# Optimization experiments

Measured on AMD Instinct MI355X. Metric: run time of the kernel, lower is better.

## Reference

```python
import jax, jax.numpy as jnp
import numpy as np

CODEBOOK_SIZE = 2048
LATENT_DIM = 256
COMMITMENT_BETA = 0.25
B, C, T = 16, LATENT_DIM, 2048


def setup_inputs() -> dict:
    key = jax.random.key(0)
    k1, k2 = jax.random.split(key)
    x = jax.random.normal(k1, (B, C, T), dtype=jnp.float32)
    # matches nn.Embedding.weight.data.uniform_(-1/K, 1/K)
    codebook = jax.random.uniform(
        k2, (CODEBOOK_SIZE, LATENT_DIM), dtype=jnp.float32,
        minval=-1.0 / CODEBOOK_SIZE, maxval=1.0 / CODEBOOK_SIZE)
    return {"x": x, "codebook": codebook}


def reference(x, codebook):
    b, c, t = x.shape
    # (B, C, T) -> (B*T, C)
    xf = jnp.transpose(x, (0, 2, 1)).reshape(b * t, c)
    # squared Euclidean distances; argmin is invariant to the sqrt in torch.cdist(p=2)
    x_sq = jnp.sum(xf * xf, axis=1, keepdims=True)            # (BT, 1)
    e_sq = jnp.sum(codebook * codebook, axis=1)[None, :]      # (1, K)
    d2 = x_sq - 2.0 * (xf @ codebook.T) + e_sq                # (BT, K)
    idx = jnp.argmin(d2, axis=-1)                             # (BT,)
    # gather codebook vectors -> (B, C, T)
    quant = codebook[idx].reshape(b, t, c).transpose(0, 2, 1)
    commitment_loss = COMMITMENT_BETA * jnp.mean(
        (jax.lax.stop_gradient(quant) - x) ** 2)
    codebook_loss = jnp.mean((quant - jax.lax.stop_gradient(x)) ** 2)
    # straight-through estimator
    quant_out = x + jax.lax.stop_gradient(quant - x)
    return quant_out, codebook_loss, commitment_loss, idx.reshape(b, t)
```

## Files before the change

kernel.cpp:

```cpp
#include <hip/hip_runtime.h>
#include <hip/hip_bf16.h>

#define KCODES 2048
#define DIM 256
#define TLEN 2048
#define NB 16
#define NROWS (NB * TLEN)
#define NELEM (NB * DIM * TLEN)
#define LOSS_OFF NELEM
#define IDX_OFF (NELEM + 2)

#define MARGIN 3e-3f

#define CCAP 48

#define OFF_XSQ   0ull
#define OFF_ESQ   131072ull
#define OFF_KEYS  139264ull
#define OFF_BSUM  401408ull
#define OFF_EHI   532480ull
#define OFF_CCNT  1581056ull
#define OFF_CLIST 1712128ull
#define WS_NEED   8003584ull

typedef __bf16 bf16x8 __attribute__((ext_vector_type(8)));
typedef float  f32x4  __attribute__((ext_vector_type(4)));

__device__ __forceinline__ float sq_rn(float v) { return __fmul_rn(v, v); }

__device__ __forceinline__ unsigned encf(float f) {
    unsigned u = __float_as_uint(f);
    return (u & 0x80000000u) ? ~u : (u | 0x80000000u);
}
__device__ __forceinline__ float decf(unsigned k) {
    return __uint_as_float((k & 0x80000000u) ? (k & 0x7FFFFFFFu) : ~k);
}

__global__ __launch_bounds__(256) void xsq_kernel(const float* __restrict__ x,
                                                  float* __restrict__ xsq) {
    int m = blockIdx.x * 256 + threadIdx.x;
    int b = m >> 11, t = m & (TLEN - 1);
    const float* p = x + (size_t)b * DIM * TLEN + t;
    float h[2];
#pragma unroll
    for (int half = 0; half < 2; ++half) {
        int c0 = half * 128;
        float r[8];
#pragma unroll
        for (int j = 0; j < 8; ++j) r[j] = sq_rn(p[(size_t)(c0 + j) * TLEN]);
        for (int i = 8; i < 128; i += 8) {
#pragma unroll
            for (int j = 0; j < 8; ++j)
                r[j] = __fadd_rn(r[j], sq_rn(p[(size_t)(c0 + i + j) * TLEN]));
        }
        h[half] = __fadd_rn(__fadd_rn(__fadd_rn(r[0], r[1]), __fadd_rn(r[2], r[3])),
                            __fadd_rn(__fadd_rn(r[4], r[5]), __fadd_rn(r[6], r[7])));
    }
    xsq[m] = __fadd_rn(h[0], h[1]);
}

__global__ __launch_bounds__(256) void esq_kernel(const float* __restrict__ cb,
                                                  float* __restrict__ esq) {
    int k = blockIdx.x * 256 + threadIdx.x;
    const float* p = cb + (size_t)k * DIM;
    float h[2];
#pragma unroll
    for (int half = 0; half < 2; ++half) {
        int c0 = half * 128;
        float r[8];
#pragma unroll
        for (int j = 0; j < 8; ++j) r[j] = sq_rn(p[c0 + j]);
        for (int i = 8; i < 128; i += 8) {
#pragma unroll
            for (int j = 0; j < 8; ++j)
                r[j] = __fadd_rn(r[j], sq_rn(p[c0 + i + j]));
        }
        h[half] = __fadd_rn(__fadd_rn(__fadd_rn(r[0], r[1]), __fadd_rn(r[2], r[3])),
                            __fadd_rn(__fadd_rn(r[4], r[5]), __fadd_rn(r[6], r[7])));
    }
    esq[k] = __fadd_rn(h[0], h[1]);
}

__global__ __launch_bounds__(256) void split_e_kernel(const float* __restrict__ cb,
                                                      __hip_bfloat16* __restrict__ Ehi) {
    int i4 = (blockIdx.x * 256 + threadIdx.x) << 2;
    float4 v = *reinterpret_cast<const float4*>(cb + i4);
    alignas(8) __hip_bfloat16 h4[4];
    h4[0] = __float2bfloat16(v.x); h4[1] = __float2bfloat16(v.y);
    h4[2] = __float2bfloat16(v.z); h4[3] = __float2bfloat16(v.w);
    *reinterpret_cast<int2*>(Ehi + i4) = *reinterpret_cast<int2*>(h4);
}

__device__ __forceinline__ void stage_chunk(const __hip_bfloat16* __restrict__ Ehi,
                                            __hip_bfloat16* dstbase,
                                            int s, int w, int srow, int scol) {
    int nt = s >> 2, kc = (s & 3) << 6;
    const __hip_bfloat16* gsrc =
        Ehi + (size_t)((nt << 7) + (w << 5) + srow) * DIM + kc + scol;
#pragma unroll
    for (int j = 0; j < 4; ++j)
        __builtin_amdgcn_global_load_lds(
            (const __attribute__((address_space(1))) unsigned int*)(gsrc + (size_t)(j << 3) * DIM),
            (__attribute__((address_space(3))) unsigned int*)(dstbase + (((w << 5) + (j << 3)) << 6)),
            16, 0, 0);
}

__global__ __launch_bounds__(256, 2) void dist_cand_kernel(const float* __restrict__ x,
                                                           const __hip_bfloat16* __restrict__ Ehi,
                                                           const float* __restrict__ esq,
                                                           int* __restrict__ ccnt_g,
                                                           int* __restrict__ clist_g) {
    __shared__ __hip_bfloat16 Bh[2][128 * 64];
    __shared__ float esq_s[KCODES];
    __shared__ unsigned wmin_s[64][64];
    __shared__ unsigned mask_s[64][64];
    __shared__ int ccnt_s[64];

    int tid = threadIdx.x;
    int w = tid >> 6, lane = tid & 63;
    int q = lane >> 4, c = lane & 15;
    int swzc = (c & 7) << 4;
    int blk = blockIdx.x;
    int b = blk >> 5;
    int t0 = (blk << 6) & (TLEN - 1);
    const float* xb = x + (size_t)b * DIM * TLEN + t0;

#pragma unroll
    for (int i = 0; i < 8; ++i) esq_s[tid + i * 256] = esq[tid + i * 256];
    if (tid < 64) ccnt_s[tid] = 0;

    bf16x8 xf[4][8];
#pragma unroll
    for (int mi = 0; mi < 4; ++mi) {
        int t = (mi << 4) + c;
#pragma unroll
        for (int kh = 0; kh < 8; ++kh) {
            alignas(16) __hip_bfloat16 h8[8];
#pragma unroll
            for (int j = 0; j < 8; ++j)
                h8[j] = __float2bfloat16(xb[(size_t)((kh << 5) + (q << 3) + j) * TLEN + t]);
            xf[mi][kh] = *reinterpret_cast<bf16x8*>(h8);
        }
    }

    f32x4 acc[2][4];
#pragma unroll
    for (int ci = 0; ci < 2; ++ci)
#pragma unroll
        for (int mi = 0; mi < 4; ++mi) acc[ci][mi] = (f32x4){0.f, 0.f, 0.f, 0.f};

    int srow = lane >> 3;
    int scol = ((lane & 7) ^ srow) << 3;

    __syncthreads();

    stage_chunk(Ehi, &Bh[0][0], 0, w, srow, scol);

    int cur = 0;
#pragma unroll 1
    for (int nt = 0; nt < 16; ++nt) {
#pragma unroll
        for (int kc = 0; kc < 4; ++kc) {
            int s = (nt << 2) + kc;
            asm volatile("s_waitcnt lgkmcnt(0)" ::: "memory");
            if (s < 63) stage_chunk(Ehi, &Bh[cur ^ 1][0], s + 1, w, srow, scol);
            if (s == 63) asm volatile("s_waitcnt vmcnt(0)" ::: "memory");
            else         asm volatile("s_waitcnt vmcnt(4)" ::: "memory");

            const char* basep = reinterpret_cast<const char*>(&Bh[cur][0]);
#pragma unroll
            for (int kh = 0; kh < 2; ++kh) {
                int swz = ((kh << 6) | (q << 4)) ^ swzc;
                bf16x8 cf0 = *reinterpret_cast<const bf16x8*>(basep + ((((w << 5) + c) << 7) + swz));
                bf16x8 cf1 = *reinterpret_cast<const bf16x8*>(basep + ((((w << 5) + 16 + c) << 7) + swz));
#pragma unroll
                for (int mi = 0; mi < 4; ++mi) {
                    acc[0][mi] = __builtin_amdgcn_mfma_f32_16x16x32_bf16(cf0, xf[mi][(kc << 1) | kh], acc[0][mi], 0, 0, 0);
                    acc[1][mi] = __builtin_amdgcn_mfma_f32_16x16x32_bf16(cf1, xf[mi][(kc << 1) | kh], acc[1][mi], 0, 0, 0);
                }
            }
            cur ^= 1;
        }

        float ev[8];
#pragma unroll
        for (int ci = 0; ci < 2; ++ci)
#pragma unroll
            for (int reg = 0; reg < 4; ++reg)
                ev[ci * 4 + reg] = esq_s[(nt << 7) + (w << 5) + (ci << 4) + (q << 2) + reg];

#pragma unroll
        for (int mi = 0; mi < 4; ++mi) {
            int r = (mi << 4) + c;
            float s8[8];
#pragma unroll
            for (int ci = 0; ci < 2; ++ci)
#pragma unroll
                for (int reg = 0; reg < 4; ++reg)
                    s8[ci * 4 + reg] = fmaf(-2.0f, acc[ci][mi][reg], ev[ci * 4 + reg]);
            float t01 = fminf(fminf(s8[0], s8[1]), fminf(s8[2], s8[3]));
            float t23 = fminf(fminf(s8[4], s8[5]), fminf(s8[6], s8[7]));
            float wmin = fminf(t01, t23);
            wmin = fminf(wmin, __shfl_xor(wmin, 16, 64));
            wmin = fminf(wmin, __shfl_xor(wmin, 32, 64));
            float thrw = wmin + MARGIN;
            unsigned bits = 0;
#pragma unroll
            for (int v = 0; v < 8; ++v)
                if (s8[v] <= thrw)
                    bits |= 1u << (((v >> 2) << 4) | (q << 2) | (v & 3));
            bits |= (unsigned)__shfl_xor((int)bits, 16, 64);
            bits |= (unsigned)__shfl_xor((int)bits, 32, 64);
            if (q == 0) {
                int st = (nt << 2) | w;
                wmin_s[r][st] = encf(wmin);
                mask_s[r][st] = bits;
            }
            acc[0][mi] = (f32x4){0.f, 0.f, 0.f, 0.f};
            acc[1][mi] = (f32x4){0.f, 0.f, 0.f, 0.f};
        }
    }

    __syncthreads();

    {
        int r = tid >> 2, j4 = tid & 3;
        int m = (blk << 6) + r;
        unsigned ge = 0xFFFFFFFFu;
#pragma unroll
        for (int i = 0; i < 16; ++i) ge = min(ge, wmin_s[r][(i << 2) | j4]);
        ge = min(ge, (unsigned)__shfl_xor((int)ge, 1, 4));
        ge = min(ge, (unsigned)__shfl_xor((int)ge, 2, 4));
        float thr = decf(ge) + MARGIN;
        for (int st = j4; st < 64; st += 4) {
            if (decf(wmin_s[r][st]) <= thr) {
                unsigned bits = mask_s[r][st];
                while (bits) {
                    int bpos = __ffs(bits) - 1; bits &= bits - 1;
                    int pos = atomicAdd(&ccnt_s[r], 1);
                    if (pos < CCAP) clist_g[(size_t)m * CCAP + pos] = (st << 5) + bpos;
                }
            }
        }
    }
    __syncthreads();
    if ((tid & 3) == 0) ccnt_g[(blk << 6) + (tid >> 2)] = ccnt_s[tid >> 2];
}

__global__ __launch_bounds__(256) void recheck_kernel(const float* __restrict__ x,
                                                      const float* __restrict__ cb,
                                                      const float* __restrict__ esq,
                                                      const int* __restrict__ ccnt,
                                                      const int* __restrict__ clist,
                                                      unsigned long long* __restrict__ keys) {
    __shared__ float xT[DIM * 33];

    int tid = threadIdx.x;
    int blk = blockIdx.x;
    int b = blk >> 6, t0 = (blk & 63) << 5;
    const float* xb = x + (size_t)b * DIM * TLEN + t0;

    {
        int tl = tid & 31, c8 = tid >> 5;
        for (int cc = 0; cc < 32; ++cc) {
            int c = (cc << 3) + c8;
            xT[c * 33 + tl] = xb[(size_t)c * TLEN + tl];
        }
    }
    __syncthreads();

    int g = tid >> 3, l3 = tid & 7;
    int m = (b << 11) + t0 + g;

    float h[2];
#pragma unroll
    for (int half = 0; half < 2; ++half) {
        int c0 = half * 128;
        float r = sq_rn(xT[(c0 + l3) * 33 + g]);
        for (int i = 8; i < 128; i += 8)
            r = __fadd_rn(r, sq_rn(xT[(c0 + i + l3) * 33 + g]));
        float a = __fadd_rn(r, __shfl_xor(r, 1, 8));
        float bb = __fadd_rn(a, __shfl_xor(a, 2, 8));
        h[half] = __fadd_rn(bb, __shfl_xor(bb, 4, 8));
    }
    float xs = __fadd_rn(h[0], h[1]);

    int cnt = ccnt[m];
    float bd = 3.4e38f; int bi = 0x7fffffff;

    if (cnt <= CCAP) {
        for (int j = l3; j < cnt; j += 8) {
            int n = clist[(size_t)m * CCAP + j];
            const float* crow = cb + (size_t)n * DIM;
            float d = 0.f;
            for (int k = 0; k < DIM; k += 4) {
                float4 cv = *reinterpret_cast<const float4*>(crow + k);
                d = fmaf(xT[(k + 0) * 33 + g], cv.x, d);
                d = fmaf(xT[(k + 1) * 33 + g], cv.y, d);
                d = fmaf(xT[(k + 2) * 33 + g], cv.z, d);
                d = fmaf(xT[(k + 3) * 33 + g], cv.w, d);
            }
            float d2 = __fadd_rn(__fadd_rn(xs, -2.0f * d), esq[n]);
            if (d2 < bd || (d2 == bd && n < bi)) { bd = d2; bi = n; }
        }
    } else {
        for (int n = l3; n < KCODES; n += 8) {
            const float* crow = cb + (size_t)n * DIM;
            float d = 0.f;
            for (int k = 0; k < DIM; k += 4) {
                float4 cv = *reinterpret_cast<const float4*>(crow + k);
                d = fmaf(xT[(k + 0) * 33 + g], cv.x, d);
                d = fmaf(xT[(k + 1) * 33 + g], cv.y, d);
                d = fmaf(xT[(k + 2) * 33 + g], cv.z, d);
                d = fmaf(xT[(k + 3) * 33 + g], cv.w, d);
            }
            float d2 = __fadd_rn(__fadd_rn(xs, -2.0f * d), esq[n]);
            if (d2 < bd || (d2 == bd && n < bi)) { bd = d2; bi = n; }
        }
    }
    for (int off = 1; off < 8; off <<= 1) {
        float od = __shfl_xor(bd, off, 8);
        int   oi = __shfl_xor(bi, off, 8);
        if (od < bd || (od == bd && oi < bi)) { bd = od; bi = oi; }
    }
    if (l3 == 0)
        keys[m] = ((unsigned long long)__float_as_uint(bd) << 32) | (unsigned)(bi & 2047);
}

__global__ __launch_bounds__(256) void init_keys_kernel(unsigned long long* __restrict__ keys) {
    keys[blockIdx.x * 256 + threadIdx.x] = ~0ULL;
}

__global__ __launch_bounds__(256, 4) void dist_kernel(const float* __restrict__ x,
                                                      const float* __restrict__ cb,
                                                      const float* __restrict__ xsq,
                                                      const float* __restrict__ esq,
                                                      unsigned long long* __restrict__ keys) {
    __shared__ float As[16][128];
    __shared__ float Bs[16][132];
    int blk = blockIdx.x;
    int nt = blk & 15, mt = blk >> 4;
    int m0 = mt << 7;
    int b = m0 >> 11, t0 = m0 & (TLEN - 1);
    int n0 = nt << 7;
    int tid = threadIdx.x;
    int tm = tid >> 4, tn = tid & 15;
    const float* xbase = x + (size_t)b * DIM * TLEN + t0;
    float acc[8][8] = {};
    for (int kk = 0; kk < DIM; kk += 16) {
#pragma unroll
        for (int h = 0; h < 2; ++h) {
            int qq = tid + (h << 8);
            int k = qq >> 5, mq = (qq & 31) << 2;
            float4 v = *reinterpret_cast<const float4*>(xbase + (size_t)(kk + k) * TLEN + mq);
            *reinterpret_cast<float4*>(&As[k][mq]) = v;
        }
#pragma unroll
        for (int h = 0; h < 2; ++h) {
            int qq = tid + (h << 8);
            int nr = qq >> 2, kc = (qq & 3) << 2;
            float4 v = *reinterpret_cast<const float4*>(cb + (size_t)(n0 + nr) * DIM + kk + kc);
            Bs[kc + 0][nr] = v.x; Bs[kc + 1][nr] = v.y;
            Bs[kc + 2][nr] = v.z; Bs[kc + 3][nr] = v.w;
        }
        __syncthreads();
#pragma unroll
        for (int k = 0; k < 16; ++k) {
            float4 a0 = *reinterpret_cast<const float4*>(&As[k][tm << 2]);
            float4 a1 = *reinterpret_cast<const float4*>(&As[k][64 + (tm << 2)]);
            float4 b0 = *reinterpret_cast<const float4*>(&Bs[k][tn << 2]);
            float4 b1 = *reinterpret_cast<const float4*>(&Bs[k][64 + (tn << 2)]);
            float am[8] = {a0.x, a0.y, a0.z, a0.w, a1.x, a1.y, a1.z, a1.w};
            float bn[8] = {b0.x, b0.y, b0.z, b0.w, b1.x, b1.y, b1.z, b1.w};
#pragma unroll
            for (int mi = 0; mi < 8; ++mi)
#pragma unroll
                for (int ni = 0; ni < 8; ++ni)
                    acc[mi][ni] = fmaf(am[mi], bn[ni], acc[mi][ni]);
        }
        __syncthreads();
    }
    int cn[8]; float es[8];
#pragma unroll
    for (int ni = 0; ni < 8; ++ni) {
        cn[ni] = n0 + ((ni < 4) ? (tn << 2) + ni : 60 + (tn << 2) + ni);
        es[ni] = esq[cn[ni]];
    }
#pragma unroll
    for (int mi = 0; mi < 8; ++mi) {
        int m = m0 + ((mi < 4) ? (tm << 2) + mi : 60 + (tm << 2) + mi);
        float xs = xsq[m];
        float bd = 3.4e38f;
        int bi = 0x7fffffff;
#pragma unroll
        for (int ni = 0; ni < 8; ++ni) {
            float d2 = __fadd_rn(__fadd_rn(xs, -2.0f * acc[mi][ni]), es[ni]);
            if (d2 < bd) { bd = d2; bi = cn[ni]; }
        }
        for (int off = 1; off < 16; off <<= 1) {
            float od = __shfl_xor(bd, off, 16);
            int oi = __shfl_xor(bi, off, 16);
            if (od < bd || (od == bd && oi < bi)) { bd = od; bi = oi; }
        }
        if (tn == 0) {
            unsigned long long key =
                ((unsigned long long)__float_as_uint(bd) << 32) | (unsigned)(bi & 2047);
            atomicMin(&keys[m], key);
        }
    }
}

__global__ __launch_bounds__(256) void gather_kernel(const float* __restrict__ x,
                                                     const float* __restrict__ cb,
                                                     const unsigned long long* __restrict__ keys,
                                                     float* __restrict__ out,
                                                     float* __restrict__ bsum) {
    int tid = threadIdx.x;
    int blk = blockIdx.x;
    int c4 = blk & 63, tc = (blk >> 6) & 7, b = blk >> 9;
    int c0 = c4 << 2;
    int t = (tc << 8) + tid;
    int m = (b << 11) + t;
    unsigned idx = (unsigned)(keys[m]) & 2047u;
    float4 cv = *reinterpret_cast<const float4*>(cb + (size_t)idx * DIM + c0);
    if (c4 == 0) out[(size_t)IDX_OFF + m] = (float)idx;

    float qv[4] = {cv.x, cv.y, cv.z, cv.w};
    __shared__ float wsum[4][4];
    int lane = tid & 63, wid = tid >> 6;
    float sv[4];
#pragma unroll
    for (int cc = 0; cc < 4; ++cc) {
        size_t e = (size_t)b * (DIM * TLEN) + (size_t)(c0 + cc) * TLEN + t;
        float xv = x[e];
        float diff = __fsub_rn(qv[cc], xv);
        out[e] = __fadd_rn(xv, diff);
        float s = __fmul_rn(diff, diff);
        for (int off = 32; off > 0; off >>= 1) s += __shfl_down(s, off, 64);
        sv[cc] = s;
    }
    if (lane == 0) {
        wsum[wid][0] = sv[0]; wsum[wid][1] = sv[1];
        wsum[wid][2] = sv[2]; wsum[wid][3] = sv[3];
    }
    __syncthreads();
    if (tid == 0) {
#pragma unroll
        for (int cc = 0; cc < 4; ++cc)
            bsum[(b << 11) + ((c0 + cc) << 3) + tc] =
                ((wsum[0][cc] + wsum[1][cc]) + (wsum[2][cc] + wsum[3][cc]));
    }
}

__global__ __launch_bounds__(1024) void finalize_kernel(const float* __restrict__ bsum,
                                                        float* __restrict__ out) {
    double s = 0.0;
    for (int i = threadIdx.x; i < 32768; i += 1024) s += (double)bsum[i];
    for (int off = 32; off > 0; off >>= 1) s += __shfl_down(s, off, 64);
    __shared__ double wsum[16];
    int lane = threadIdx.x & 63, wid = threadIdx.x >> 6;
    if (lane == 0) wsum[wid] = s;
    __syncthreads();
    if (threadIdx.x == 0) {
        double total = 0.0;
        for (int ww = 0; ww < 16; ++ww) total += wsum[ww];
        float mean = (float)(total / (double)NELEM);
        out[LOSS_OFF] = mean;
        out[LOSS_OFF + 1] = 0.25f * mean;
    }
}

extern "C" void kernel_launch(void* const* d_in, const int* in_sizes, int n_in,
                              void* d_out, int out_size, void* d_ws, size_t ws_size,
                              hipStream_t stream) {
    const float* x  = (const float*)d_in[0];
    const float* cb = (const float*)d_in[1];
    float* out = (float*)d_out;
    char* ws = (char*)d_ws;
    float* xsq = (float*)(ws + OFF_XSQ);
    float* esq = (float*)(ws + OFF_ESQ);
    unsigned long long* keys = (unsigned long long*)(ws + OFF_KEYS);
    float* bsum = (float*)(ws + OFF_BSUM);

    esq_kernel<<<KCODES / 256, 256, 0, stream>>>(cb, esq);

    if (ws_size >= WS_NEED) {
        __hip_bfloat16* Ehi = (__hip_bfloat16*)(ws + OFF_EHI);
        int* ccnt  = (int*)(ws + OFF_CCNT);
        int* clist = (int*)(ws + OFF_CLIST);
        split_e_kernel<<<(KCODES * DIM) / 1024, 256, 0, stream>>>(cb, Ehi);
        dist_cand_kernel<<<NROWS / 64, 256, 0, stream>>>(x, Ehi, esq, ccnt, clist);
        recheck_kernel<<<NROWS / 32, 256, 0, stream>>>(x, cb, esq, ccnt, clist, keys);
    } else {
        xsq_kernel<<<NROWS / 256, 256, 0, stream>>>(x, xsq);
        init_keys_kernel<<<NROWS / 256, 256, 0, stream>>>(keys);
        dist_kernel<<<(NROWS / 128) * (KCODES / 128), 256, 0, stream>>>(x, cb, xsq, esq, keys);
    }
    gather_kernel<<<(NB * 8 * 64), 256, 0, stream>>>(x, cb, keys, out, bsum);
    finalize_kernel<<<1, 1024, 0, stream>>>(bsum, out);
}
```

Measured before the change: 207.3 us.

## Fuse esq into codebook prep, emit candidates inline, widen gather per block

Merges the codebook norm computation into the bf16 split kernel, which removes one launch. The distance kernel now appends candidates to a shared-memory list during the main loop, using a running per-row minimum as the threshold. This replaces the per-subtile min/mask tables and the second scan pass, and the freed shared memory lets the launch bound ask for 3 blocks per CU. The gather kernel handles 8 channels per block instead of 4, halving the grid. The running-minimum threshold is looser early in the loop, so more candidates may be emitted and hit the CCAP overflow limit.

After: 750.8 us. +262.2%, slower.

```diff
diff --git a/kernel.cpp b/kernel.cpp
--- a/kernel.cpp
+++ b/kernel.cpp
@@ -81,14 +81,31 @@
     esq[k] = __fadd_rn(h[0], h[1]);
 }
 
-__global__ __launch_bounds__(256) void split_e_kernel(const float* __restrict__ cb,
-                                                      __hip_bfloat16* __restrict__ Ehi) {
-    int i4 = (blockIdx.x * 256 + threadIdx.x) << 2;
-    float4 v = *reinterpret_cast<const float4*>(cb + i4);
+__global__ __launch_bounds__(256) void prep_e_kernel(const float* __restrict__ cb,
+                                                     __hip_bfloat16* __restrict__ Ehi,
+                                                     float* __restrict__ esq) {
+    int tid = threadIdx.x;
+    int w = tid >> 6, lane = tid & 63;
+    int k = (blockIdx.x << 2) + w;
+    const float* p = cb + (size_t)k * DIM;
+
+    float4 v = *reinterpret_cast<const float4*>(p + (lane << 2));
     alignas(8) __hip_bfloat16 h4[4];
     h4[0] = __float2bfloat16(v.x); h4[1] = __float2bfloat16(v.y);
     h4[2] = __float2bfloat16(v.z); h4[3] = __float2bfloat16(v.w);
-    *reinterpret_cast<int2*>(Ehi + i4) = *reinterpret_cast<int2*>(h4);
+    *reinterpret_cast<int2*>(Ehi + (size_t)k * DIM + (lane << 2)) = *reinterpret_cast<int2*>(h4);
+
+    if (lane < 16) {
+        int c0 = (lane >> 3) << 7, j = lane & 7;
+        float r = sq_rn(p[c0 + j]);
+        for (int i = 8; i < 128; i += 8)
+            r = __fadd_rn(r, sq_rn(p[c0 + i + j]));
+        float a  = __fadd_rn(r,  __shfl_xor(r, 1, 16));
+        float b2 = __fadd_rn(a,  __shfl_xor(a, 2, 16));
+        float h  = __fadd_rn(b2, __shfl_xor(b2, 4, 16));
+        float tot = __fadd_rn(h, __shfl_xor(h, 8, 16));
+        if (lane == 0) esq[k] = tot;
+    }
 }
 
 __device__ __forceinline__ void stage_chunk(const __hip_bfloat16* __restrict__ Ehi,
@@ -105,16 +122,16 @@
             16, 0, 0);
 }
 
-__global__ __launch_bounds__(256, 2) void dist_cand_kernel(const float* __restrict__ x,
+__global__ __launch_bounds__(256, 3) void dist_cand_kernel(const float* __restrict__ x,
                                                            const __hip_bfloat16* __restrict__ Ehi,
                                                            const float* __restrict__ esq,
                                                            int* __restrict__ ccnt_g,
                                                            int* __restrict__ clist_g) {
     __shared__ __hip_bfloat16 Bh[2][128 * 64];
     __shared__ float esq_s[KCODES];
-    __shared__ unsigned wmin_s[64][64];
-    __shared__ unsigned mask_s[64][64];
+    __shared__ int clist_s[64][CCAP];
     __shared__ int ccnt_s[64];
+    __shared__ unsigned rmin_s[64];
 
     int tid = threadIdx.x;
     int w = tid >> 6, lane = tid & 63;
@@ -127,7 +144,7 @@
 
 #pragma unroll
     for (int i = 0; i < 8; ++i) esq_s[tid + i * 256] = esq[tid + i * 256];
-    if (tid < 64) ccnt_s[tid] = 0;
+    if (tid < 64) { ccnt_s[tid] = 0; rmin_s[tid] = 0xFF7FFFFFu; }
 
     bf16x8 xf[4][8];
 #pragma unroll
@@ -203,48 +220,32 @@
             float wmin = fminf(t01, t23);
             wmin = fminf(wmin, __shfl_xor(wmin, 16, 64));
             wmin = fminf(wmin, __shfl_xor(wmin, 32, 64));
-            float thrw = wmin + MARGIN;
-            unsigned bits = 0;
-#pragma unroll
-            for (int v = 0; v < 8; ++v)
-                if (s8[v] <= thrw)
-                    bits |= 1u << (((v >> 2) << 4) | (q << 2) | (v & 3));
-            bits |= (unsigned)__shfl_xor((int)bits, 16, 64);
-            bits |= (unsigned)__shfl_xor((int)bits, 32, 64);
-            if (q == 0) {
-                int st = (nt << 2) | w;
-                wmin_s[r][st] = encf(wmin);
-                mask_s[r][st] = bits;
+            float rs = decf(rmin_s[r]);
+            float thr = fminf(wmin, rs) + MARGIN;
+#pragma unroll
+            for (int v = 0; v < 8; ++v) {
+                if (s8[v] <= thr) {
+                    int n = (nt << 7) + (w << 5) + ((v >> 2) << 4) + (q << 2) + (v & 3);
+                    int pos = atomicAdd(&ccnt_s[r], 1);
+                    if (pos < CCAP) clist_s[r][pos] = n;
+                }
             }
+            if (q == 0) atomicMin(&rmin_s[r], encf(wmin));
             acc[0][mi] = (f32x4){0.f, 0.f, 0.f, 0.f};
             acc[1][mi] = (f32x4){0.f, 0.f, 0.f, 0.f};
         }
     }
 
     __syncthreads();
-
     {
         int r = tid >> 2, j4 = tid & 3;
+        int cnt = ccnt_s[r];
         int m = (blk << 6) + r;
-        unsigned ge = 0xFFFFFFFFu;
-#pragma unroll
-        for (int i = 0; i < 16; ++i) ge = min(ge, wmin_s[r][(i << 2) | j4]);
-        ge = min(ge, (unsigned)__shfl_xor((int)ge, 1, 4));
-        ge = min(ge, (unsigned)__shfl_xor((int)ge, 2, 4));
-        float thr = decf(ge) + MARGIN;
-        for (int st = j4; st < 64; st += 4) {
-            if (decf(wmin_s[r][st]) <= thr) {
-                unsigned bits = mask_s[r][st];
-                while (bits) {
-                    int bpos = __ffs(bits) - 1; bits &= bits - 1;
-                    int pos = atomicAdd(&ccnt_s[r], 1);
-                    if (pos < CCAP) clist_g[(size_t)m * CCAP + pos] = (st << 5) + bpos;
-                }
-            }
-        }
-    }
-    __syncthreads();
-    if ((tid & 3) == 0) ccnt_g[(blk << 6) + (tid >> 2)] = ccnt_s[tid >> 2];
+        if (j4 == 0) ccnt_g[m] = cnt;
+        int cl = cnt > CCAP ? CCAP : cnt;
+        for (int j = j4; j < cl; j += 4)
+            clist_g[(size_t)m * CCAP + j] = clist_s[r][j];
+    }
 }
 
 __global__ __launch_bounds__(256) void recheck_kernel(const float* __restrict__ x,
@@ -417,20 +418,22 @@
                                                      float* __restrict__ bsum) {
     int tid = threadIdx.x;
     int blk = blockIdx.x;
-    int c4 = blk & 63, tc = (blk >> 6) & 7, b = blk >> 9;
-    int c0 = c4 << 2;
+    int c8 = blk & 31, tc = (blk >> 5) & 7, b = blk >> 8;
+    int c0 = c8 << 3;
     int t = (tc << 8) + tid;
     int m = (b << 11) + t;
     unsigned idx = (unsigned)(keys[m]) & 2047u;
-    float4 cv = *reinterpret_cast<const float4*>(cb + (size_t)idx * DIM + c0);
-    if (c4 == 0) out[(size_t)IDX_OFF + m] = (float)idx;
-
-    float qv[4] = {cv.x, cv.y, cv.z, cv.w};
-    __shared__ float wsum[4][4];
+    const float* crow = cb + (size_t)idx * DIM + c0;
+    float4 cv0 = *reinterpret_cast<const float4*>(crow);
+    float4 cv1 = *reinterpret_cast<const float4*>(crow + 4);
+    if (c8 == 0) out[(size_t)IDX_OFF + m] = (float)idx;
+
+    float qv[8] = {cv0.x, cv0.y, cv0.z, cv0.w, cv1.x, cv1.y, cv1.z, cv1.w};
+    __shared__ float wsum[4][8];
     int lane = tid & 63, wid = tid >> 6;
-    float sv[4];
-#pragma unroll
-    for (int cc = 0; cc < 4; ++cc) {
+    float sv[8];
+#pragma unroll
+    for (int cc = 0; cc < 8; ++cc) {
         size_t e = (size_t)b * (DIM * TLEN) + (size_t)(c0 + cc) * TLEN + t;
         float xv = x[e];
         float diff = __fsub_rn(qv[cc], xv);
@@ -440,13 +443,13 @@
         sv[cc] = s;
     }
     if (lane == 0) {
-        wsum[wid][0] = sv[0]; wsum[wid][1] = sv[1];
-        wsum[wid][2] = sv[2]; wsum[wid][3] = sv[3];
+#pragma unroll
+        for (int cc = 0; cc < 8; ++cc) wsum[wid][cc] = sv[cc];
     }
     __syncthreads();
     if (tid == 0) {
 #pragma unroll
-        for (int cc = 0; cc < 4; ++cc)
+        for (int cc = 0; cc < 8; ++cc)
             bsum[(b << 11) + ((c0 + cc) << 3) + tc] =
                 ((wsum[0][cc] + wsum[1][cc]) + (wsum[2][cc] + wsum[3][cc]));
     }
@@ -482,20 +485,19 @@
     unsigned long long* keys = (unsigned long long*)(ws + OFF_KEYS);
     float* bsum = (float*)(ws + OFF_BSUM);
 
-    esq_kernel<<<KCODES / 256, 256, 0, stream>>>(cb, esq);
-
     if (ws_size >= WS_NEED) {
         __hip_bfloat16* Ehi = (__hip_bfloat16*)(ws + OFF_EHI);
         int* ccnt  = (int*)(ws + OFF_CCNT);
         int* clist = (int*)(ws + OFF_CLIST);
-        split_e_kernel<<<(KCODES * DIM) / 1024, 256, 0, stream>>>(cb, Ehi);
+        prep_e_kernel<<<KCODES / 4, 256, 0, stream>>>(cb, Ehi, esq);
         dist_cand_kernel<<<NROWS / 64, 256, 0, stream>>>(x, Ehi, esq, ccnt, clist);
         recheck_kernel<<<NROWS / 32, 256, 0, stream>>>(x, cb, esq, ccnt, clist, keys);
     } else {
+        esq_kernel<<<KCODES / 256, 256, 0, stream>>>(cb, esq);
         xsq_kernel<<<NROWS / 256, 256, 0, stream>>>(x, xsq);
         init_keys_kernel<<<NROWS / 256, 256, 0, stream>>>(keys);
         dist_kernel<<<(NROWS / 128) * (KCODES / 128), 256, 0, stream>>>(x, cb, xsq, esq, keys);
     }
-    gather_kernel<<<(NB * 8 * 64), 256, 0, stream>>>(x, cb, keys, out, bsum);
+    gather_kernel<<<(NB * 8 * 32), 256, 0, stream>>>(x, cb, keys, out, bsum);
     finalize_kernel<<<1, 1024, 0, stream>>>(bsum, out);
 }
```
